# Kernel optimization log

Measured on AMD Instinct MI355X. Metric: run time of the kernel, lower is better.

The kernel has to match this reference:

```python
import jax, jax.numpy as jnp
import numpy as np


def setup_inputs() -> dict:
    key = jax.random.key(0)
    ks = jax.random.split(key, 6)
    B, C, S = 256, 2048, 7          # batch, embed_dim, spacial_dim
    OUT = 1024                      # output_dim
    return {
        "x": jax.random.normal(ks[0], (B, C, S, S), jnp.float32),
        "pos_emb": jax.random.normal(ks[1], (S * S + 1, C), jnp.float32) / (C ** 0.5),
        "Wv": jax.random.normal(ks[2], (C, C), jnp.float32) * 0.02,
        "bv": jnp.zeros((C,), jnp.float32),
        "Wc": jax.random.normal(ks[3], (OUT, C), jnp.float32) * 0.02,
        "bc": jnp.zeros((OUT,), jnp.float32),
        "num_heads": 32,
    }


def reference(x, pos_emb, Wv, bv, Wc, bc, num_heads):
    # x: [B, C, H, W] -> tokens [B, HW, C], prepend mean token -> [B, N, C]
    B, C, H, W = x.shape
    N = H * W + 1
    hd = C // num_heads
    scale = hd ** -0.5

    t = x.reshape(B, C, H * W).transpose(0, 2, 1)                    # [B, HW, C]
    t = jnp.concatenate([t.mean(axis=1, keepdims=True), t], axis=1)  # [B, N, C]
    t = t + pos_emb[None]                                            # add pos emb

    # qkv weights are all copies of v_proj => q = k = v = v_proj(t)
    v = t @ Wv.T + bv                                                # [B, N, C]
    vh = v.reshape(B, N, num_heads, hd).transpose(0, 2, 1, 3)        # [B, h, N, d]

    # attn_ori = softmax(q k^T * scale) with q=k=v; dropout p=0 (eval)
    attn = jax.nn.softmax(jnp.einsum('bhnd,bhmd->bhnm', vh, vh) * scale, axis=-1)
    ctx = jnp.einsum('bhnm,bhmd->bhnd', attn, vh)                    # [B, h, N, d]
    ctx = ctx.transpose(0, 2, 1, 3).reshape(B, N, C)

    # proj weights come from c_proj: [out_dim, C]
    x_ori = ctx @ Wc.T + bc                                          # [B, N, out]
    xout = v @ Wc.T + bc                                             # x-path: proj(v) directly
    # x[:, 0, :] = x_ori[:, 0, :]; module returns x (first list element)
    return xout.at[:, 0, :].set(x_ori[:, 0, :])
```

## Files before the change

### kernel.cpp

```cpp
#include <hip/hip_runtime.h>
#include <stdint.h>

#define BATCH  256
#define CDIM   2048
#define HW     49
#define NTOK   50
#define MROWS  (BATCH * NTOK)
#define ODIM   1024
#define NHEADS 32

typedef __attribute__((ext_vector_type(8))) short short8;
typedef __attribute__((ext_vector_type(4))) float f32x4;
typedef unsigned short u16;
typedef unsigned int   u32;

__device__ __forceinline__ float bf2f(u16 u) {
  union { u32 i; float f; } v; v.i = ((u32)u) << 16; return v.f;
}
__device__ __forceinline__ u16 f2bf(float f) {
  union { float f; u32 i; } v; v.f = f;
  u32 r = v.i + 0x7fffu + ((v.i >> 16) & 1u);
  return (u16)(r >> 16);
}

__device__ __forceinline__ void async16(const void* g, void* l) {
  __builtin_amdgcn_global_load_lds(
      (const __attribute__((address_space(1))) u32*)g,
      (__attribute__((address_space(3))) u32*)l, 16, 0, 0);
}

__global__ __launch_bounds__(256) void cvt_kernel(const float* __restrict__ in,
                                                  u16* __restrict__ out, int n4) {
  int i = blockIdx.x * 256 + threadIdx.x;
  if (i >= n4) return;
  float4 v = reinterpret_cast<const float4*>(in)[i];
  ushort4 o;
  o.x = f2bf(v.x); o.y = f2bf(v.y); o.z = f2bf(v.z); o.w = f2bf(v.w);
  reinterpret_cast<ushort4*>(out)[i] = o;
}

__global__ __launch_bounds__(256) void prep_kernel(const float* __restrict__ x,
                                                   const float* __restrict__ pos,
                                                   u16* __restrict__ T) {
  const int blk = blockIdx.x;
  const int b  = blk >> 5;
  const int c0 = (blk & 31) * 64;
  __shared__ float xs[64 * HW];
  __shared__ float mean[64];
  const float* src = x + ((size_t)b * CDIM + c0) * HW;
  for (int i = threadIdx.x; i < 64 * HW; i += 256) xs[i] = src[i];
  __syncthreads();
  if (threadIdx.x < 64) {
    float s = 0.f;
#pragma unroll
    for (int j = 0; j < HW; j++) s += xs[threadIdx.x * HW + j];
    mean[threadIdx.x] = s * (1.0f / 49.0f);
  }
  __syncthreads();
  for (int wi = threadIdx.x; wi < NTOK * 8; wi += 256) {
    const int n = wi >> 3;
    const int g = (wi & 7) * 8;
    alignas(16) u16 ov[8];
#pragma unroll
    for (int u = 0; u < 8; u++) {
      const int c = g + u;
      float val = (n == 0) ? mean[c] : xs[c * HW + (n - 1)];
      val += pos[n * CDIM + c0 + c];
      ov[u] = f2bf(val);
    }
    *reinterpret_cast<uint4*>(&T[((size_t)b * NTOK + n) * CDIM + c0 + g]) =
        *reinterpret_cast<const uint4*>(ov);
  }
}

template<int OUT_BF16>
__global__ __launch_bounds__(512, 2)
void gemm256(const u16* __restrict__ A, const u16* __restrict__ Bm,
             const float* __restrict__ bias, void* __restrict__ Cout,
             int M, int N, int K, int nbx) {
  __shared__ __align__(16) u16 smem[65536];

  const int NK = K >> 6;
  const int t = threadIdx.x;
  const int lane = t & 63;
  const int wid = t >> 6;
  const int wm = wid >> 2;
  const int wn = wid & 3;

  const int nwg = gridDim.x;
  const int cpx = nwg >> 3;
  const int orig = blockIdx.x;
  const int swz = (orig & 7) * cpx + (orig >> 3);
  const int bx = swz % nbx;
  const int by = swz / nbx;
  const int m0 = by * 256, n0 = bx * 256;

  const int tr  = t >> 3;
  const int to8 = ((t & 7) ^ (tr & 7)) << 3;
  const int t8  = t << 3;
  const u16* pA0 = A  + (size_t)(m0 + tr) * K + to8;
  const u16* pB0 = Bm + (size_t)(n0 + tr) * K + to8;

  const int lr = lane & 15, hi = lane >> 4;
  const int sx = lr & 7;
  const int aK0 = ((wm * 128 + lr) << 6) + (((0 + hi) ^ sx) << 3);
  const int aK1 = ((wm * 128 + lr) << 6) + (((4 + hi) ^ sx) << 3);
  const int bK0 = 16384 + ((wn * 64 + lr) << 6) + (((0 + hi) ^ sx) << 3);
  const int bK1 = 16384 + ((wn * 64 + lr) << 6) + (((4 + hi) ^ sx) << 3);

  f32x4 acc[8][4] = {};
  short8 af[8][2], bf[4][2];

  auto STAGE = [&](int s) {
    if (s < 4 * NK) {
      const int kti = s >> 2;
      const int isB = (s >> 1) & 1;
      const int h   = s & 1;
      const u16* g = (isB ? pB0 : pA0) + (size_t)(h * 128) * K + kti * 64;
      u16* l = &smem[((kti & 1) << 15) + (isB << 14) + (h << 13) + t8];
      async16(g, l);
      async16(g + (size_t)64 * K, l + 4096);
    }
  };

#pragma unroll
  for (int s = 0; s < 6; ++s) STAGE(s);
  asm volatile("s_waitcnt vmcnt(4)" ::: "memory");
  __builtin_amdgcn_s_barrier();

  for (int j = 0; j < NK; ++j) {
    const u16* sa = &smem[(j & 1) << 15];

#pragma unroll
    for (int f = 0; f < 4; ++f) {
      af[f][0] = *(const short8*)&sa[aK0 + f * 1024];
      af[f][1] = *(const short8*)&sa[aK1 + f * 1024];
    }
#pragma unroll
    for (int f = 0; f < 2; ++f) {
      bf[f][0] = *(const short8*)&sa[bK0 + f * 1024];
      bf[f][1] = *(const short8*)&sa[bK1 + f * 1024];
    }
    STAGE(4 * j + 6);
    __builtin_amdgcn_s_barrier();
    asm volatile("s_waitcnt lgkmcnt(0)" ::: "memory");
    __builtin_amdgcn_sched_barrier(0);
    __builtin_amdgcn_s_setprio(1);
#pragma unroll
    for (int fm = 0; fm < 4; ++fm)
#pragma unroll
      for (int fn = 0; fn < 2; ++fn) {
        acc[fm][fn] = __builtin_amdgcn_mfma_f32_16x16x32_bf16(af[fm][0], bf[fn][0], acc[fm][fn], 0, 0, 0);
        acc[fm][fn] = __builtin_amdgcn_mfma_f32_16x16x32_bf16(af[fm][1], bf[fn][1], acc[fm][fn], 0, 0, 0);
      }
    __builtin_amdgcn_s_setprio(0);
    __builtin_amdgcn_s_barrier();

#pragma unroll
    for (int f = 4; f < 8; ++f) {
      af[f][0] = *(const short8*)&sa[aK0 + f * 1024];
      af[f][1] = *(const short8*)&sa[aK1 + f * 1024];
    }
#pragma unroll
    for (int f = 2; f < 4; ++f) {
      bf[f][0] = *(const short8*)&sa[bK0 + f * 1024];
      bf[f][1] = *(const short8*)&sa[bK1 + f * 1024];
    }
    STAGE(4 * j + 7);
    __builtin_amdgcn_s_barrier();
    asm volatile("s_waitcnt lgkmcnt(0)" ::: "memory");
    __builtin_amdgcn_sched_barrier(0);
    __builtin_amdgcn_s_setprio(1);
#pragma unroll
    for (int fm = 4; fm < 8; ++fm)
#pragma unroll
      for (int fn = 0; fn < 2; ++fn) {
        acc[fm][fn] = __builtin_amdgcn_mfma_f32_16x16x32_bf16(af[fm][0], bf[fn][0], acc[fm][fn], 0, 0, 0);
        acc[fm][fn] = __builtin_amdgcn_mfma_f32_16x16x32_bf16(af[fm][1], bf[fn][1], acc[fm][fn], 0, 0, 0);
      }
    __builtin_amdgcn_s_setprio(0);
    __builtin_amdgcn_s_barrier();

    STAGE(4 * j + 8);
    __builtin_amdgcn_s_barrier();
    __builtin_amdgcn_s_setprio(1);
#pragma unroll
    for (int fm = 0; fm < 4; ++fm)
#pragma unroll
      for (int fn = 2; fn < 4; ++fn) {
        acc[fm][fn] = __builtin_amdgcn_mfma_f32_16x16x32_bf16(af[fm][0], bf[fn][0], acc[fm][fn], 0, 0, 0);
        acc[fm][fn] = __builtin_amdgcn_mfma_f32_16x16x32_bf16(af[fm][1], bf[fn][1], acc[fm][fn], 0, 0, 0);
      }
    __builtin_amdgcn_s_setprio(0);
    __builtin_amdgcn_s_barrier();

    STAGE(4 * j + 9);
    __builtin_amdgcn_s_barrier();
    __builtin_amdgcn_s_setprio(1);
#pragma unroll
    for (int fm = 4; fm < 8; ++fm)
#pragma unroll
      for (int fn = 2; fn < 4; ++fn) {
        acc[fm][fn] = __builtin_amdgcn_mfma_f32_16x16x32_bf16(af[fm][0], bf[fn][0], acc[fm][fn], 0, 0, 0);
        acc[fm][fn] = __builtin_amdgcn_mfma_f32_16x16x32_bf16(af[fm][1], bf[fn][1], acc[fm][fn], 0, 0, 0);
      }
    __builtin_amdgcn_s_setprio(0);
    if (j < NK - 2) asm volatile("s_waitcnt vmcnt(4)" ::: "memory");
    else            asm volatile("s_waitcnt vmcnt(0)" ::: "memory");
    __builtin_amdgcn_s_barrier();
  }

  const int erow = hi * 4;
#pragma unroll
  for (int fm = 0; fm < 8; ++fm) {
#pragma unroll
    for (int fn = 0; fn < 4; ++fn) {
      const int cg = n0 + wn * 64 + fn * 16 + lr;
      const float bb = bias[cg];
      const int rbase = m0 + wm * 128 + fm * 16 + erow;
#pragma unroll
      for (int jr = 0; jr < 4; ++jr) {
        const float val = acc[fm][fn][jr] + bb;
        if (OUT_BF16)
          ((u16*)Cout)[(size_t)(rbase + jr) * N + cg] = f2bf(val);
        else
          ((float*)Cout)[(size_t)(rbase + jr) * N + cg] = val;
      }
    }
  }
}

__global__ __launch_bounds__(64) void attn0_kernel(u16* __restrict__ V) {
  const int b = blockIdx.x, h = blockIdx.y;
  __shared__ __align__(16) u16 vt[NTOK * 64];
  __shared__ float pb[64];
  const int t = threadIdx.x;
  u16* base = V + (size_t)b * NTOK * CDIM + h * 64;
  for (int idx = t; idx < NTOK * 8; idx += 64) {
    const int m = idx >> 3, g = (idx & 7) * 8;
    *reinterpret_cast<uint4*>(&vt[m * 64 + g]) =
        *reinterpret_cast<const uint4*>(base + (size_t)m * CDIM + g);
  }
  __syncthreads();
  const float qd = bf2f(vt[t]);
  float s_own = -1e30f;
  for (int m = 0; m < NTOK; m++) {
    float p = qd * bf2f(vt[m * 64 + t]);
#pragma unroll
    for (int off = 32; off; off >>= 1) p += __shfl_xor(p, off);
    if (t == m) s_own = p * 0.125f;
  }
  float mx = s_own;
#pragma unroll
  for (int off = 32; off; off >>= 1) mx = fmaxf(mx, __shfl_xor(mx, off));
  const float e = (t < NTOK) ? __expf(s_own - mx) : 0.f;
  float Z = e;
#pragma unroll
  for (int off = 32; off; off >>= 1) Z += __shfl_xor(Z, off);
  pb[t] = e / Z;
  __syncthreads();
  float acc = 0.f;
  for (int m = 0; m < NTOK; m++) acc += pb[m] * bf2f(vt[m * 64 + t]);
  base[t] = f2bf(acc);
}

extern "C" void kernel_launch(void* const* d_in, const int* in_sizes, int n_in,
                              void* d_out, int out_size, void* d_ws, size_t ws_size,
                              hipStream_t stream) {
  const float* x   = (const float*)d_in[0];
  const float* pos = (const float*)d_in[1];
  const float* Wv  = (const float*)d_in[2];
  const float* bv  = (const float*)d_in[3];
  const float* Wc  = (const float*)d_in[4];
  const float* bc  = (const float*)d_in[5];
  float* out = (float*)d_out;

  u16* T   = (u16*)d_ws;
  u16* V   = T   + (size_t)MROWS * CDIM;
  u16* WvB = V   + (size_t)MROWS * CDIM;
  u16* WcB = WvB + (size_t)CDIM * CDIM;

  {
    int n4 = CDIM * CDIM / 4;
    cvt_kernel<<<(n4 + 255) / 256, 256, 0, stream>>>(Wv, WvB, n4);
  }
  {
    int n4 = ODIM * CDIM / 4;
    cvt_kernel<<<(n4 + 255) / 256, 256, 0, stream>>>(Wc, WcB, n4);
  }
  prep_kernel<<<BATCH * 32, 256, 0, stream>>>(x, pos, T);

  gemm256<1><<<(MROWS / 256) * (CDIM / 256), 512, 0, stream>>>(
      T, WvB, bv, V, MROWS, CDIM, CDIM, CDIM / 256);

  attn0_kernel<<<dim3(BATCH, NHEADS), 64, 0, stream>>>(V);

  gemm256<0><<<(MROWS / 256) * (ODIM / 256), 512, 0, stream>>>(
      V, WcB, bc, out, MROWS, ODIM, CDIM, ODIM / 256);
}
```

Measured before the change: 309.9 us.

## Reorder GEMM MFMA quadrants to halve fragment registers and merge weight conversions

```diff
diff --git a/kernel.cpp b/kernel.cpp
--- a/kernel.cpp
+++ b/kernel.cpp
@@ -29,14 +29,22 @@
       (__attribute__((address_space(3))) u32*)l, 16, 0, 0);
 }
 
-__global__ __launch_bounds__(256) void cvt_kernel(const float* __restrict__ in,
-                                                  u16* __restrict__ out, int n4) {
+__global__ __launch_bounds__(256) void cvt2_kernel(const float* __restrict__ a,
+                                                   u16* __restrict__ oa, int n4a,
+                                                   const float* __restrict__ bsrc,
+                                                   u16* __restrict__ ob, int n4b) {
   int i = blockIdx.x * 256 + threadIdx.x;
-  if (i >= n4) return;
-  float4 v = reinterpret_cast<const float4*>(in)[i];
+  const float* src; u16* dst; int idx;
+  if (i < n4a) { src = a; dst = oa; idx = i; }
+  else {
+    idx = i - n4a;
+    if (idx >= n4b) return;
+    src = bsrc; dst = ob;
+  }
+  float4 v = reinterpret_cast<const float4*>(src)[idx];
   ushort4 o;
   o.x = f2bf(v.x); o.y = f2bf(v.y); o.z = f2bf(v.z); o.w = f2bf(v.w);
-  reinterpret_cast<ushort4*>(out)[i] = o;
+  reinterpret_cast<ushort4*>(dst)[idx] = o;
 }
 
 __global__ __launch_bounds__(256) void prep_kernel(const float* __restrict__ x,
@@ -109,13 +117,10 @@
   const int bK1 = 16384 + ((wn * 64 + lr) << 6) + (((4 + hi) ^ sx) << 3);
 
   f32x4 acc[8][4] = {};
-  short8 af[8][2], bf[4][2];
-
-  auto STAGE = [&](int s) {
-    if (s < 4 * NK) {
-      const int kti = s >> 2;
-      const int isB = (s >> 1) & 1;
-      const int h   = s & 1;
+  short8 a[4][2], b[2][2];
+
+  auto STG = [&](int kti, int isB, int h) {
+    if (kti < NK) {
       const u16* g = (isB ? pB0 : pA0) + (size_t)(h * 128) * K + kti * 64;
       u16* l = &smem[((kti & 1) << 15) + (isB << 14) + (h << 13) + t8];
       async16(g, l);
@@ -123,9 +128,8 @@
     }
   };
 
-#pragma unroll
-  for (int s = 0; s < 6; ++s) STAGE(s);
-  asm volatile("s_waitcnt vmcnt(4)" ::: "memory");
+  STG(0, 0, 0); STG(0, 0, 1); STG(0, 1, 0); STG(0, 1, 1); STG(1, 0, 0);
+  asm volatile("s_waitcnt vmcnt(2)" ::: "memory");
   __builtin_amdgcn_s_barrier();
 
   for (int j = 0; j < NK; ++j) {
@@ -133,15 +137,15 @@
 
 #pragma unroll
     for (int f = 0; f < 4; ++f) {
-      af[f][0] = *(const short8*)&sa[aK0 + f * 1024];
-      af[f][1] = *(const short8*)&sa[aK1 + f * 1024];
+      a[f][0] = *(const short8*)&sa[aK0 + f * 1024];
+      a[f][1] = *(const short8*)&sa[aK1 + f * 1024];
     }
 #pragma unroll
     for (int f = 0; f < 2; ++f) {
-      bf[f][0] = *(const short8*)&sa[bK0 + f * 1024];
-      bf[f][1] = *(const short8*)&sa[bK1 + f * 1024];
-    }
-    STAGE(4 * j + 6);
+      b[f][0] = *(const short8*)&sa[bK0 + f * 1024];
+      b[f][1] = *(const short8*)&sa[bK1 + f * 1024];
+    }
+    STG(j + 1, 0, 1);
     __builtin_amdgcn_s_barrier();
     asm volatile("s_waitcnt lgkmcnt(0)" ::: "memory");
     __builtin_amdgcn_sched_barrier(0);
@@ -150,62 +154,71 @@
     for (int fm = 0; fm < 4; ++fm)
 #pragma unroll
       for (int fn = 0; fn < 2; ++fn) {
-        acc[fm][fn] = __builtin_amdgcn_mfma_f32_16x16x32_bf16(af[fm][0], bf[fn][0], acc[fm][fn], 0, 0, 0);
-        acc[fm][fn] = __builtin_amdgcn_mfma_f32_16x16x32_bf16(af[fm][1], bf[fn][1], acc[fm][fn], 0, 0, 0);
+        acc[fm][fn] = __builtin_amdgcn_mfma_f32_16x16x32_bf16(a[fm][0], b[fn][0], acc[fm][fn], 0, 0, 0);
+        acc[fm][fn] = __builtin_amdgcn_mfma_f32_16x16x32_bf16(a[fm][1], b[fn][1], acc[fm][fn], 0, 0, 0);
       }
     __builtin_amdgcn_s_setprio(0);
     __builtin_amdgcn_s_barrier();
 
 #pragma unroll
-    for (int f = 4; f < 8; ++f) {
-      af[f][0] = *(const short8*)&sa[aK0 + f * 1024];
-      af[f][1] = *(const short8*)&sa[aK1 + f * 1024];
-    }
-#pragma unroll
-    for (int f = 2; f < 4; ++f) {
-      bf[f][0] = *(const short8*)&sa[bK0 + f * 1024];
-      bf[f][1] = *(const short8*)&sa[bK1 + f * 1024];
-    }
-    STAGE(4 * j + 7);
+    for (int f = 0; f < 2; ++f) {
+      b[f][0] = *(const short8*)&sa[bK0 + (2 + f) * 1024];
+      b[f][1] = *(const short8*)&sa[bK1 + (2 + f) * 1024];
+    }
+    STG(j + 1, 1, 0);
     __builtin_amdgcn_s_barrier();
     asm volatile("s_waitcnt lgkmcnt(0)" ::: "memory");
     __builtin_amdgcn_sched_barrier(0);
     __builtin_amdgcn_s_setprio(1);
 #pragma unroll
-    for (int fm = 4; fm < 8; ++fm)
+    for (int fm = 0; fm < 4; ++fm)
 #pragma unroll
       for (int fn = 0; fn < 2; ++fn) {
-        acc[fm][fn] = __builtin_amdgcn_mfma_f32_16x16x32_bf16(af[fm][0], bf[fn][0], acc[fm][fn], 0, 0, 0);
-        acc[fm][fn] = __builtin_amdgcn_mfma_f32_16x16x32_bf16(af[fm][1], bf[fn][1], acc[fm][fn], 0, 0, 0);
+        acc[fm][2 + fn] = __builtin_amdgcn_mfma_f32_16x16x32_bf16(a[fm][0], b[fn][0], acc[fm][2 + fn], 0, 0, 0);
+        acc[fm][2 + fn] = __builtin_amdgcn_mfma_f32_16x16x32_bf16(a[fm][1], b[fn][1], acc[fm][2 + fn], 0, 0, 0);
       }
     __builtin_amdgcn_s_setprio(0);
     __builtin_amdgcn_s_barrier();
 
-    STAGE(4 * j + 8);
-    __builtin_amdgcn_s_barrier();
+#pragma unroll
+    for (int f = 0; f < 4; ++f) {
+      a[f][0] = *(const short8*)&sa[aK0 + (4 + f) * 1024];
+      a[f][1] = *(const short8*)&sa[aK1 + (4 + f) * 1024];
+    }
+    STG(j + 1, 1, 1);
+    __builtin_amdgcn_s_barrier();
+    asm volatile("s_waitcnt lgkmcnt(0)" ::: "memory");
+    __builtin_amdgcn_sched_barrier(0);
     __builtin_amdgcn_s_setprio(1);
 #pragma unroll
     for (int fm = 0; fm < 4; ++fm)
 #pragma unroll
-      for (int fn = 2; fn < 4; ++fn) {
-        acc[fm][fn] = __builtin_amdgcn_mfma_f32_16x16x32_bf16(af[fm][0], bf[fn][0], acc[fm][fn], 0, 0, 0);
-        acc[fm][fn] = __builtin_amdgcn_mfma_f32_16x16x32_bf16(af[fm][1], bf[fn][1], acc[fm][fn], 0, 0, 0);
+      for (int fn = 0; fn < 2; ++fn) {
+        acc[4 + fm][2 + fn] = __builtin_amdgcn_mfma_f32_16x16x32_bf16(a[fm][0], b[fn][0], acc[4 + fm][2 + fn], 0, 0, 0);
+        acc[4 + fm][2 + fn] = __builtin_amdgcn_mfma_f32_16x16x32_bf16(a[fm][1], b[fn][1], acc[4 + fm][2 + fn], 0, 0, 0);
       }
     __builtin_amdgcn_s_setprio(0);
     __builtin_amdgcn_s_barrier();
 
-    STAGE(4 * j + 9);
-    __builtin_amdgcn_s_barrier();
+#pragma unroll
+    for (int f = 0; f < 2; ++f) {
+      b[f][0] = *(const short8*)&sa[bK0 + f * 1024];
+      b[f][1] = *(const short8*)&sa[bK1 + f * 1024];
+    }
+    STG(j + 2, 0, 0);
+    __builtin_amdgcn_s_barrier();
+    asm volatile("s_waitcnt lgkmcnt(0)" ::: "memory");
+    __builtin_amdgcn_sched_barrier(0);
     __builtin_amdgcn_s_setprio(1);
 #pragma unroll
-    for (int fm = 4; fm < 8; ++fm)
-#pragma unroll
-      for (int fn = 2; fn < 4; ++fn) {
-        acc[fm][fn] = __builtin_amdgcn_mfma_f32_16x16x32_bf16(af[fm][0], bf[fn][0], acc[fm][fn], 0, 0, 0);
-        acc[fm][fn] = __builtin_amdgcn_mfma_f32_16x16x32_bf16(af[fm][1], bf[fn][1], acc[fm][fn], 0, 0, 0);
+    for (int fm = 0; fm < 4; ++fm)
+#pragma unroll
+      for (int fn = 0; fn < 2; ++fn) {
+        acc[4 + fm][fn] = __builtin_amdgcn_mfma_f32_16x16x32_bf16(a[fm][0], b[fn][0], acc[4 + fm][fn], 0, 0, 0);
+        acc[4 + fm][fn] = __builtin_amdgcn_mfma_f32_16x16x32_bf16(a[fm][1], b[fn][1], acc[4 + fm][fn], 0, 0, 0);
       }
     __builtin_amdgcn_s_setprio(0);
-    if (j < NK - 2) asm volatile("s_waitcnt vmcnt(4)" ::: "memory");
+    if (j < NK - 2) asm volatile("s_waitcnt vmcnt(2)" ::: "memory");
     else            asm volatile("s_waitcnt vmcnt(0)" ::: "memory");
     __builtin_amdgcn_s_barrier();
   }
@@ -281,12 +294,9 @@
   u16* WcB = WvB + (size_t)CDIM * CDIM;
 
   {
-    int n4 = CDIM * CDIM / 4;
-    cvt_kernel<<<(n4 + 255) / 256, 256, 0, stream>>>(Wv, WvB, n4);
-  }
-  {
-    int n4 = ODIM * CDIM / 4;
-    cvt_kernel<<<(n4 + 255) / 256, 256, 0, stream>>>(Wc, WcB, n4);
+    int n4a = CDIM * CDIM / 4;
+    int n4b = ODIM * CDIM / 4;
+    cvt2_kernel<<<(n4a + n4b + 255) / 256, 256, 0, stream>>>(Wv, WvB, n4a, Wc, WcB, n4b);
   }
   prep_kernel<<<BATCH * 32, 256, 0, stream>>>(x, pos, T);
 
```

New measurement: 310.5 us. No clear change (+0.2%).
